# Kernel tuning notes

Hardware: AMD Instinct MI355X
Metric: run time of the kernel (lower is better)

Reference implementation:

```python
import jax, jax.numpy as jnp
import numpy as np

DIM = 512
HEADS = 8
DIM_HEAD = 64
LANDMARKS = 256  # dim // 2
PINV_ITERS = 6
KERNEL = 33  # residual conv kernel
NUM_LAYERS = 2
NUM_CLASSES = 2


def layernorm(x, g, b, eps=1e-5):
    mu = x.mean(-1, keepdims=True)
    var = ((x - mu) ** 2).mean(-1, keepdims=True)
    return (x - mu) * jax.lax.rsqrt(var + eps) * g + b


def moore_penrose_pinv(x, iters=PINV_ITERS):
    # x: (b, h, m, m); scaling uses GLOBAL max over all batch/heads (torch.max)
    abs_x = jnp.abs(x)
    col = abs_x.sum(-1).max()
    row = abs_x.sum(-2).max()
    z = jnp.swapaxes(x, -1, -2) / (col * row)
    I = jnp.eye(x.shape[-1], dtype=x.dtype)
    for _ in range(iters):
        xz = x @ z
        z = 0.25 * z @ (13. * I - xz @ (15. * I - xz @ (7. * I - xz)))
    return z


def nystrom_attention(x, w_qkv, w_out, b_out, conv_w):
    # x: (b, n, dim)
    b, n, _ = x.shape
    m = LANDMARKS
    pad = (m - n % m) % m
    if pad:
        x = jnp.pad(x, ((0, 0), (pad, 0), (0, 0)))  # pad at FRONT
    nf = n + pad
    qkv = x @ w_qkv  # (b, nf, 3*h*dh)
    qkv = qkv.reshape(b, nf, 3, HEADS, DIM_HEAD)
    q = jnp.transpose(qkv[:, :, 0], (0, 2, 1, 3)) * (DIM_HEAD ** -0.5)  # (b,h,nf,dh)
    k = jnp.transpose(qkv[:, :, 1], (0, 2, 1, 3))
    v = jnp.transpose(qkv[:, :, 2], (0, 2, 1, 3))
    l = nf // m
    q_l = q.reshape(b, HEADS, m, l, DIM_HEAD).mean(3)  # (b,h,m,dh)
    k_l = k.reshape(b, HEADS, m, l, DIM_HEAD).mean(3)
    sim1 = jnp.einsum('bhid,bhjd->bhij', q, k_l)      # (b,h,nf,m)
    sim2 = jnp.einsum('bhid,bhjd->bhij', q_l, k_l)    # (b,h,m,m)
    sim3 = jnp.einsum('bhid,bhjd->bhij', q_l, k)      # (b,h,m,nf)
    attn1 = jax.nn.softmax(sim1, axis=-1)
    attn2 = jax.nn.softmax(sim2, axis=-1)
    attn3 = jax.nn.softmax(sim3, axis=-1)
    attn2_inv = moore_penrose_pinv(attn2)
    out = (attn1 @ attn2_inv) @ (attn3 @ v)  # (b,h,nf,dh)
    # residual depthwise conv over sequence dim, per head (Conv2d groups=heads)
    res = jax.lax.conv_general_dilated(
        v, conv_w, window_strides=(1, 1), padding=((KERNEL // 2, KERNEL // 2), (0, 0)),
        dimension_numbers=('NCHW', 'OIHW', 'NCHW'), feature_group_count=HEADS)
    out = out + res
    out = jnp.transpose(out, (0, 2, 1, 3)).reshape(b, nf, HEADS * DIM_HEAD)
    out = out @ w_out + b_out
    return out[:, -n:]


def setup_inputs() -> dict:
    key = jax.random.key(0)
    ks = jax.random.split(key, 16)
    B, N = 2, 8191
    s = 0.02
    inp = {
        'h': jax.random.normal(ks[0], (B, N, 1024), jnp.float32),
        'w1': jax.random.normal(ks[1], (1024, DIM), jnp.float32) * s,
        'b1': jnp.zeros((DIM,), jnp.float32),
        'cls_token': jax.random.normal(ks[2], (1, 1, DIM), jnp.float32),
        'ln_g': jnp.ones((NUM_LAYERS, DIM), jnp.float32),
        'ln_b': jnp.zeros((NUM_LAYERS, DIM), jnp.float32),
        'w_qkv': jax.random.normal(ks[3], (NUM_LAYERS, DIM, 3 * HEADS * DIM_HEAD), jnp.float32) * s,
        'w_out': jax.random.normal(ks[4], (NUM_LAYERS, HEADS * DIM_HEAD, DIM), jnp.float32) * s,
        'b_out': jnp.zeros((NUM_LAYERS, DIM), jnp.float32),
        'conv_w': jax.random.normal(ks[5], (NUM_LAYERS, HEADS, 1, KERNEL, 1), jnp.float32) * s,
        'fn_g': jnp.ones((DIM,), jnp.float32),
        'fn_b': jnp.zeros((DIM,), jnp.float32),
        'w2': jax.random.normal(ks[6], (DIM, NUM_CLASSES), jnp.float32) * s,
        'b2': jnp.zeros((NUM_CLASSES,), jnp.float32),
    }
    return inp


def reference(h, w1, b1, cls_token, ln_g, ln_b, w_qkv, w_out, b_out, conv_w, fn_g, fn_b, w2, b2):
    x = jax.nn.relu(h @ w1 + b1)  # (B,N,512)
    B = x.shape[0]
    cls = jnp.broadcast_to(cls_token, (B, 1, DIM))
    x = jnp.concatenate([cls, x], axis=1)  # (B, N+1, 512)
    for i in range(NUM_LAYERS):
        x = x + nystrom_attention(layernorm(x, ln_g[i], ln_b[i]), w_qkv[i], w_out[i], b_out[i], conv_w[i])
    x = layernorm(x, fn_g, fn_b)[:, 0]
    logits = x @ w2 + b2
    return logits
```

## Files before the change

kernel.cpp:

```cpp
#include <hip/hip_runtime.h>
#include <hip/hip_bf16.h>

#define DIM 512
#define HEADS 8
#define DH 64
#define LM 256
#define NF 8192
#define BHN 16

typedef __attribute__((ext_vector_type(8))) short short8;
typedef __attribute__((ext_vector_type(4))) float f32x4;

__device__ __forceinline__ float bf2f(unsigned short u) {
  return __uint_as_float((unsigned)u << 16);
}
__device__ __forceinline__ unsigned short f2bf(float x) {
  unsigned u = __float_as_uint(x);
  unsigned r = u + 0x7fffu + ((u >> 16) & 1u);
  return (unsigned short)(r >> 16);
}

__device__ __forceinline__ void gl2lds16(const void* g, void* l) {
  __builtin_amdgcn_global_load_lds(
      (const __attribute__((address_space(1))) void*)g,
      (__attribute__((address_space(3))) void*)l, 16, 0, 0);
}

__device__ __forceinline__ void lds_fence() {
  asm volatile("s_waitcnt lgkmcnt(0)" ::: "memory");
  __builtin_amdgcn_sched_barrier(0);
}

__device__ __forceinline__ float waveReduceSum(float v) {
#pragma unroll
  for (int o = 1; o < 64; o <<= 1) v += __shfl_xor(v, o);
  return v;
}
__device__ __forceinline__ float waveReduceMax(float v) {
#pragma unroll
  for (int o = 1; o < 64; o <<= 1) v = fmaxf(v, __shfl_xor(v, o));
  return v;
}
__device__ __forceinline__ float blockReduceSum256(float v, float* sm) {
  v = waveReduceSum(v);
  int w = threadIdx.x >> 6;
  __syncthreads();
  if ((threadIdx.x & 63) == 0) sm[w] = v;
  __syncthreads();
  return sm[0] + sm[1] + sm[2] + sm[3];
}
__device__ __forceinline__ float blockReduceMax256(float v, float* sm) {
  v = waveReduceMax(v);
  int w = threadIdx.x >> 6;
  __syncthreads();
  if ((threadIdx.x & 63) == 0) sm[w] = v;
  __syncthreads();
  return fmaxf(fmaxf(sm[0], sm[1]), fmaxf(sm[2], sm[3]));
}

__global__ __launch_bounds__(256)
void cvt_bf16(const float* __restrict__ in, unsigned short* __restrict__ out,
              long long n) {
  long long i = ((long long)blockIdx.x * 256 + threadIdx.x) * 4;
  if (i + 3 < n) {
    float4 v = *(const float4*)&in[i];
    ushort4 o;
    o.x = f2bf(v.x); o.y = f2bf(v.y); o.z = f2bf(v.z); o.w = f2bf(v.w);
    *(ushort4*)&out[i] = o;
  } else {
    for (; i < n; i++) out[i] = f2bf(in[i]);
  }
}

__global__ __launch_bounds__(256)
void cvt_transpose(const float* __restrict__ in, unsigned short* __restrict__ out,
                   int Kd, int Nd) {
  __shared__ float t[32][33];
  int x = threadIdx.x & 31, y = threadIdx.x >> 5;
#pragma unroll
  for (int i = 0; i < 32; i += 8) {
    int k = blockIdx.y * 32 + y + i, n = blockIdx.x * 32 + x;
    t[y + i][x] = in[(long long)k * Nd + n];
  }
  __syncthreads();
#pragma unroll
  for (int i = 0; i < 32; i += 8) {
    int n = blockIdx.x * 32 + y + i, k = blockIdx.y * 32 + x;
    out[(long long)n * Kd + k] = f2bf(t[x][y + i]);
  }
}

__global__ __launch_bounds__(256)
void vt_transpose(const unsigned short* __restrict__ VB,
                  unsigned short* __restrict__ VT) {
  __shared__ unsigned short t[64][80];
  int bh = blockIdx.x >> 7, tile = blockIdx.x & 127;
  int n0 = tile * 64;
  int tid = threadIdx.x;
#pragma unroll
  for (int it = 0; it < 2; it++) {
    int s = it * 256 + tid;
    int nl = s >> 3, sg = s & 7;
    *(short8*)&t[nl][sg * 8] =
        *(const short8*)&VB[((long long)bh * NF + n0 + nl) * DH + sg * 8];
  }
  __syncthreads();
#pragma unroll
  for (int it = 0; it < 2; it++) {
    int s = it * 256 + tid;
    int dl = s >> 3, sg = s & 7;
    short8 v;
#pragma unroll
    for (int j = 0; j < 8; j++) ((unsigned short*)&v)[j] = t[sg * 8 + j][dl];
    *(short8*)&VT[((long long)bh * DH + dl) * NF + n0 + sg * 8] = v;
  }
}

__global__ __launch_bounds__(256) void write_cls(const float* __restrict__ cls,
                                                 float* __restrict__ X) {
  int t = blockIdx.x * 256 + threadIdx.x;
  int b = t >> 9, c = t & 511;
  X[(long long)b * NF * DIM + c] = cls[c];
}

#define MG_RELU 1
#define MG_ADDC 2
#define MG_BIAS 4
__global__ __launch_bounds__(256)
void gemm_mfma(const unsigned short* __restrict__ A,
               const unsigned short* __restrict__ B,
               const float* __restrict__ bias, float* __restrict__ C,
               unsigned short* __restrict__ qkv, unsigned short* __restrict__ vbuf,
               int M, int N, int K, int flags, int remap) {
  __shared__ short8 smem[1024];
  short8 (*Als)[64] = (short8 (*)[64])smem;
  short8 (*Bls)[64] = (short8 (*)[64])(smem + 512);
  const int tid = threadIdx.x;
  const int lane = tid & 63, wave = tid >> 6;
  const int wm = wave >> 1, wn = wave & 1;
  const int m0 = blockIdx.y * 128, n0 = blockIdx.x * 128;
  const int r16 = lane & 15, quad = lane >> 4;
  const unsigned short* pa0 = A + (long long)(m0 + 32 * wave + r16) * K + quad * 8;
  const unsigned short* pa1 = A + (long long)(m0 + 32 * wave + 16 + r16) * K + quad * 8;
  const unsigned short* pb0 = B + (long long)(n0 + 32 * wave + r16) * K + quad * 8;
  const unsigned short* pb1 = B + (long long)(n0 + 32 * wave + 16 + r16) * K + quad * 8;
  f32x4 acc[4][4] = {};
  for (int k0 = 0; k0 < K; k0 += 32) {
    gl2lds16(pa0, &Als[2 * wave][0]);
    gl2lds16(pa1, &Als[2 * wave + 1][0]);
    gl2lds16(pb0, &Bls[2 * wave][0]);
    gl2lds16(pb1, &Bls[2 * wave + 1][0]);
    pa0 += 32; pa1 += 32; pb0 += 32; pb1 += 32;
    __syncthreads();
    short8 af[4], bfr[4];
#pragma unroll
    for (int mt = 0; mt < 4; mt++) af[mt] = Als[wm * 4 + mt][lane];
#pragma unroll
    for (int nt = 0; nt < 4; nt++) bfr[nt] = Bls[wn * 4 + nt][lane];
#pragma unroll
    for (int mt = 0; mt < 4; mt++)
#pragma unroll
      for (int nt = 0; nt < 4; nt++)
        acc[mt][nt] = __builtin_amdgcn_mfma_f32_16x16x32_bf16(
            af[mt], bfr[nt], acc[mt][nt], 0, 0, 0);
    __syncthreads();
  }
  if (remap == 2) {
    unsigned short (*Ep)[32][64] = (unsigned short (*)[32][64])smem;
    int gn_base = n0 + wn * 64;
    int s = gn_base >> 9, hh = (gn_base >> 6) & 7;
    float scale = (s == 0) ? 0.125f : 1.f;
    unsigned short* basep =
        (s == 0) ? qkv : (s == 1) ? qkv + (long long)BHN * NF * DH : vbuf;
#pragma unroll
    for (int half = 0; half < 2; half++) {
      lds_fence();
#pragma unroll
      for (int mt = half * 2; mt < half * 2 + 2; mt++)
#pragma unroll
        for (int nt = 0; nt < 4; nt++)
#pragma unroll
          for (int r = 0; r < 4; r++)
            Ep[wave][(mt & 1) * 16 + quad * 4 + r][nt * 16 + r16] =
                f2bf(acc[mt][nt][r] * scale);
      lds_fence();
#pragma unroll
      for (int it = 0; it < 4; it++) {
        int idx = it * 64 + lane;
        int m_l = idx >> 3, sg = idx & 7;
        int gm = m0 + wm * 64 + half * 32 + m_l;
        int b = gm >> 13, n = gm & (NF - 1);
        int bh = b * HEADS + hh;
        short8 v = *(short8*)&Ep[wave][m_l][sg * 8];
        *(short8*)&basep[((long long)bh * NF + n) * DH + sg * 8] = v;
      }
    }
  } else {
#pragma unroll
    for (int mt = 0; mt < 4; mt++) {
#pragma unroll
      for (int nt = 0; nt < 4; nt++) {
#pragma unroll
        for (int r = 0; r < 4; r++) {
          int gm = m0 + wm * 64 + mt * 16 + quad * 4 + r;
          int gn = n0 + wn * 64 + nt * 16 + r16;
          if (gm >= M) continue;
          float v = acc[mt][nt][r];
          if (flags & MG_BIAS) v += bias[gn];
          long long idx;
          if (remap == 1) {
            int b = gm / 8191;
            int n = gm - b * 8191;
            idx = ((long long)(b * NF + 1 + n)) * DIM + gn;
          } else {
            idx = (long long)gm * N + gn;
          }
          if (flags & MG_ADDC) v += C[idx];
          if (flags & MG_RELU) v = fmaxf(v, 0.f);
          C[idx] = v;
        }
      }
    }
  }
}

__global__ __launch_bounds__(256)
void flash_attn1(const unsigned short* __restrict__ QB,
                 const unsigned short* __restrict__ KLB,
                 const unsigned short* __restrict__ WmB,
                 const unsigned short* __restrict__ XNC,
                 unsigned short* __restrict__ XNB2) {
  __shared__ unsigned short Plds[4][16][136];
  const int bh = blockIdx.y, b = bh >> 3, hh = bh & 7;
  const int tid = threadIdx.x, lane = tid & 63, wave = tid >> 6;
  const int r16 = lane & 15, quad = lane >> 4;
  const int m0w = blockIdx.x * 64 + wave * 16;
  const unsigned short* Aq = QB + (long long)bh * NF * DH;
  const unsigned short* Bk = KLB + (long long)bh * LM * DH;
  const unsigned short* Wm = WmB + (long long)bh * DH * LM;
  short8 af[2];
#pragma unroll
  for (int kc = 0; kc < 2; kc++)
    af[kc] = *(const short8*)&Aq[(long long)(m0w + r16) * DH + kc * 32 + quad * 8];
  short8 ones;
#pragma unroll
  for (int j = 0; j < 8; j++) ((unsigned short*)&ones)[j] = 0x3F80;
  f32x4 O[4] = {};
  f32x4 Ls = {};
#pragma unroll
  for (int t = 0; t < 2; t++) {
    int c0 = t * 128;
    f32x4 S[8] = {};
    __builtin_amdgcn_s_setprio(1);
#pragma unroll
    for (int nt = 0; nt < 8; nt++) {
#pragma unroll
      for (int kc = 0; kc < 2; kc++) {
        short8 bb = *(const short8*)&Bk[(long long)(c0 + nt * 16 + r16) * DH +
                                        kc * 32 + quad * 8];
        S[nt] = __builtin_amdgcn_mfma_f32_16x16x32_bf16(af[kc], bb, S[nt], 0, 0, 0);
      }
    }
    __builtin_amdgcn_s_setprio(0);
#pragma unroll
    for (int nt = 0; nt < 8; nt++)
#pragma unroll
      for (int r = 0; r < 4; r++)
        Plds[wave][quad * 4 + r][nt * 16 + r16] = f2bf(__expf(S[nt][r]));
    lds_fence();
    __builtin_amdgcn_s_setprio(1);
#pragma unroll
    for (int kc = 0; kc < 4; kc++) {
      short8 a = *(short8*)&Plds[wave][r16][kc * 32 + quad * 8];
      Ls = __builtin_amdgcn_mfma_f32_16x16x32_bf16(a, ones, Ls, 0, 0, 0);
#pragma unroll
      for (int nt2 = 0; nt2 < 4; nt2++) {
        short8 bb = *(const short8*)&Wm[(long long)(nt2 * 16 + r16) * LM + c0 +
                                        kc * 32 + quad * 8];
        O[nt2] = __builtin_amdgcn_mfma_f32_16x16x32_bf16(a, bb, O[nt2], 0, 0, 0);
      }
    }
    __builtin_amdgcn_s_setprio(0);
  }
  float invl[4];
#pragma unroll
  for (int r = 0; r < 4; r++) invl[r] = 1.f / Ls[r];
#pragma unroll
  for (int nt2 = 0; nt2 < 4; nt2++)
#pragma unroll
    for (int r = 0; r < 4; r++) {
      int row = m0w + quad * 4 + r;
      int d = nt2 * 16 + r16;
      long long gi = ((long long)(b * NF + row)) * DIM + hh * DH + d;
      XNB2[gi] = f2bf(O[nt2][r] * invl[r] + bf2f(XNC[gi]));
    }
}

__global__ __launch_bounds__(256)
void flash_attn3(const unsigned short* __restrict__ QLB,
                 const unsigned short* __restrict__ KB,
                 const unsigned short* __restrict__ VT,
                 float* __restrict__ Opart, float* __restrict__ Lpart) {
  __shared__ unsigned short Plds[4][16][136];
  const int bh = blockIdx.z, ks = blockIdx.y;
  const int tid = threadIdx.x, lane = tid & 63, wave = tid >> 6;
  const int r16 = lane & 15, quad = lane >> 4;
  const int m0w = blockIdx.x * 64 + wave * 16;
  const unsigned short* Aq = QLB + (long long)bh * LM * DH;
  const unsigned short* Bk = KB + (long long)bh * NF * DH;
  const unsigned short* Vt = VT + (long long)bh * DH * NF;
  short8 af[2];
#pragma unroll
  for (int kc = 0; kc < 2; kc++)
    af[kc] = *(const short8*)&Aq[(long long)(m0w + r16) * DH + kc * 32 + quad * 8];
  short8 ones;
#pragma unroll
  for (int j = 0; j < 8; j++) ((unsigned short*)&ones)[j] = 0x3F80;
  f32x4 O[4] = {};
  f32x4 Ls = {};
  for (int t = 0; t < 4; t++) {
    int kv0 = ks * 512 + t * 128;
    f32x4 S[8] = {};
    __builtin_amdgcn_s_setprio(1);
#pragma unroll
    for (int nt = 0; nt < 8; nt++) {
#pragma unroll
      for (int kc = 0; kc < 2; kc++) {
        short8 bb = *(const short8*)&Bk[(long long)(kv0 + nt * 16 + r16) * DH +
                                        kc * 32 + quad * 8];
        S[nt] = __builtin_amdgcn_mfma_f32_16x16x32_bf16(af[kc], bb, S[nt], 0, 0, 0);
      }
    }
    __builtin_amdgcn_s_setprio(0);
#pragma unroll
    for (int nt = 0; nt < 8; nt++)
#pragma unroll
      for (int r = 0; r < 4; r++)
        Plds[wave][quad * 4 + r][nt * 16 + r16] = f2bf(__expf(S[nt][r]));
    lds_fence();
    __builtin_amdgcn_s_setprio(1);
#pragma unroll
    for (int kc2 = 0; kc2 < 4; kc2++) {
      short8 a = *(short8*)&Plds[wave][r16][kc2 * 32 + quad * 8];
      Ls = __builtin_amdgcn_mfma_f32_16x16x32_bf16(a, ones, Ls, 0, 0, 0);
#pragma unroll
      for (int nt2 = 0; nt2 < 4; nt2++) {
        short8 bb = *(const short8*)&Vt[(long long)(nt2 * 16 + r16) * NF + kv0 +
                                        kc2 * 32 + quad * 8];
        O[nt2] = __builtin_amdgcn_mfma_f32_16x16x32_bf16(a, bb, O[nt2], 0, 0, 0);
      }
    }
    __builtin_amdgcn_s_setprio(0);
  }
  float* Ob = Opart + (((long long)ks * BHN + bh) * LM) * DH;
#pragma unroll
  for (int nt2 = 0; nt2 < 4; nt2++)
#pragma unroll
    for (int r = 0; r < 4; r++) {
      int row = m0w + quad * 4 + r;
      Ob[(long long)row * DH + nt2 * 16 + r16] = O[nt2][r];
    }
  if (r16 == 0) {
#pragma unroll
    for (int r = 0; r < 4; r++) {
      int row = m0w + quad * 4 + r;
      Lpart[((long long)ks * BHN + bh) * LM + row] = Ls[r];
    }
  }
}

__global__ __launch_bounds__(256)
void attn3_merge(const float* __restrict__ Opart, const float* __restrict__ Lpart,
                 float* __restrict__ O3) {
  int idx = blockIdx.x * 256 + threadIdx.x;
  int bh = idx >> 14, rem = idx & 16383;
  int row = rem >> 6, d = rem & 63;
  float L = 0.f, acc = 0.f;
#pragma unroll
  for (int c = 0; c < 16; c++) {
    L += Lpart[((long long)c * BHN + bh) * LM + row];
    acc += Opart[(((long long)c * BHN + bh) * LM + row) * DH + d];
  }
  O3[((long long)bh * LM + row) * DH + d] = acc / L;
}

__global__ __launch_bounds__(256)
void zinit(const float* __restrict__ a2, const unsigned* __restrict__ red,
           unsigned short* __restrict__ zn, unsigned short* __restrict__ zt) {
  float scale = 1.0f / __uint_as_float(red[1]);
  long long idx = (long long)blockIdx.x * 256 + threadIdx.x;
  int bh = (int)(idx >> 16);
  int ij = (int)(idx & 65535);
  int i = ij >> 8, j = ij & 255;
  zn[idx] = f2bf(a2[((long long)bh << 16) + (j << 8) + i] * scale);
  zt[idx] = f2bf(a2[idx] * scale);
}

#define PV_CN 1
#define PV_CT 2
#define PV_CF 4
#define PV_ID 8
__global__ __launch_bounds__(256)
void pinv_bf(const unsigned short* __restrict__ An,
             const unsigned short* __restrict__ Bt,
             unsigned short* __restrict__ Cn, unsigned short* __restrict__ Ct,
             float* __restrict__ Cf, float alpha, float ident, float beta,
             int flags) {
  __shared__ unsigned short Als[32][256];
  __shared__ unsigned short Bls[32][256];
  const int batch = blockIdx.z;
  An += (long long)batch * 65536;
  Bt += (long long)batch * 65536;
  const int tid = threadIdx.x, lane = tid & 63, wave = tid >> 6;
  const int wm2 = wave >> 1, wn2 = wave & 1;
  const int m0 = blockIdx.y * 32, n0 = blockIdx.x * 32;
  const int r16 = lane & 15, quad = lane >> 4;
#pragma unroll
  for (int j = 0; j < 4; j++) {
    int g = (j * 4 + wave) * 64 + lane;
    int row = g >> 5, plog = (g & 31) ^ (row & 7);
    gl2lds16(An + ((m0 + row) << 8) + plog * 8,
             (char*)Als + (j * 4 + wave) * 1024);
    gl2lds16(Bt + ((n0 + row) << 8) + plog * 8,
             (char*)Bls + (j * 4 + wave) * 1024);
  }
  __syncthreads();
  f32x4 acc = {};
  const int arow = wm2 * 16 + r16, brow = wn2 * 16 + r16;
#pragma unroll
  for (int kk = 0; kk < 8; kk++) {
    short8 af = *(const short8*)((const char*)Als + arow * 512 +
                                 ((kk * 4 + quad) ^ (arow & 7)) * 16);
    short8 bfr = *(const short8*)((const char*)Bls + brow * 512 +
                                  ((kk * 4 + quad) ^ (brow & 7)) * 16);
    acc = __builtin_amdgcn_mfma_f32_16x16x32_bf16(af, bfr, acc, 0, 0, 0);
  }
  long long cb = (long long)batch * 65536;
  int ncol = n0 + wn2 * 16 + r16;
  float vals[4];
#pragma unroll
  for (int r = 0; r < 4; r++) {
    int mrow = wm2 * 16 + quad * 4 + r;
    float v = beta * acc[r];
    if (flags & PV_ID) {
      unsigned short a = *(const unsigned short*)(
          (const char*)Als + mrow * 512 +
          (((ncol >> 3) ^ (mrow & 7)) * 16) + (ncol & 7) * 2);
      v += ident * bf2f(a);
    }
    vals[r] = v * alpha;
    int gm = m0 + mrow;
    if (flags & PV_CN) Cn[cb + ((long long)gm << 8) + ncol] = f2bf(vals[r]);
    if (flags & PV_CF) Cf[cb + ((long long)gm << 8) + ncol] = vals[r];
  }
  if (flags & PV_CT) {
    ushort4 o;
    o.x = f2bf(vals[0]); o.y = f2bf(vals[1]);
    o.z = f2bf(vals[2]); o.w = f2bf(vals[3]);
    *(ushort4*)&Ct[cb + ((long long)ncol << 8) + m0 + wm2 * 16 + quad * 4] = o;
  }
}

#define BG_BIDENT 16
__global__ __launch_bounds__(256)
void bgemm(const float* __restrict__ A, const float* __restrict__ B,
           float* __restrict__ C, int M, int N, int K,
           long long sA, long long sB, long long sC,
           float alpha, float ident, int flags) {
  const int batch = blockIdx.z;
  A += (long long)batch * sA;
  B += (long long)batch * sB;
  float* Cb = C + (long long)batch * sC;
  __shared__ float As[16][68];
  __shared__ float Bs[16][68];
  const int tid = threadIdx.x;
  const int tx = tid & 15, ty = tid >> 4;
  const int m0 = blockIdx.y * 64, n0 = blockIdx.x * 64;
  float acc[4][4] = {};
  for (int k0 = 0; k0 < K; k0 += 16) {
    {
      int k = tid & 15;
      int mBase = tid >> 4;
#pragma unroll
      for (int i = 0; i < 4; i++) {
        int m = mBase + i * 16;
        int gm = m0 + m;
        As[k][m] = (gm < M) ? A[(long long)gm * K + (k0 + k)] : 0.f;
      }
    }
    {
      int n = tid & 63;
      int kBase = tid >> 6;
#pragma unroll
      for (int i = 0; i < 4; i++) {
        int k = kBase + i * 4;
        int gn = n0 + n;
        float vb = (gn < N) ? B[(long long)(k0 + k) * N + gn] : 0.f;
        if (flags & BG_BIDENT) vb = ident * ((k0 + k) == gn ? 1.f : 0.f) - vb;
        Bs[k][n] = vb;
      }
    }
    __syncthreads();
#pragma unroll
    for (int k = 0; k < 16; k++) {
      float a[4], b[4];
#pragma unroll
      for (int i = 0; i < 4; i++) a[i] = As[k][ty * 4 + i];
#pragma unroll
      for (int j = 0; j < 4; j++) b[j] = Bs[k][tx * 4 + j];
#pragma unroll
      for (int i = 0; i < 4; i++)
#pragma unroll
        for (int j = 0; j < 4; j++) acc[i][j] = fmaf(a[i], b[j], acc[i][j]);
    }
    __syncthreads();
  }
#pragma unroll
  for (int i = 0; i < 4; i++) {
    int gm = m0 + ty * 4 + i;
    if (gm >= M) continue;
#pragma unroll
    for (int j = 0; j < 4; j++) {
      int gn = n0 + tx * 4 + j;
      if (gn >= N) continue;
      Cb[(long long)gm * N + gn] = alpha * acc[i][j];
    }
  }
}

__global__ __launch_bounds__(256)
void wm_gemm(const float* __restrict__ Z, const float* __restrict__ O3,
             unsigned short* __restrict__ WmT) {
  const int batch = blockIdx.y;
  const int m0 = blockIdx.x * 64;
  const float* A = Z + (long long)batch * 65536;
  const float* B = O3 + (long long)batch * LM * DH;
  __shared__ float As[16][68];
  __shared__ float Bs[16][68];
  const int tid = threadIdx.x, tx = tid & 15, ty = tid >> 4;
  float acc[4][4] = {};
  for (int k0 = 0; k0 < 256; k0 += 16) {
    {
      int k = tid & 15, mB = tid >> 4;
#pragma unroll
      for (int i = 0; i < 4; i++) {
        int m = mB + i * 16;
        As[k][m] = A[(long long)(m0 + m) * 256 + k0 + k];
      }
    }
    {
      int n = tid & 63, kB = tid >> 6;
#pragma unroll
      for (int i = 0; i < 4; i++) {
        int k = kB + i * 4;
        Bs[k][n] = B[(long long)(k0 + k) * DH + n];
      }
    }
    __syncthreads();
#pragma unroll
    for (int k = 0; k < 16; k++) {
      float a[4], b[4];
#pragma unroll
      for (int i = 0; i < 4; i++) a[i] = As[k][ty * 4 + i];
#pragma unroll
      for (int j = 0; j < 4; j++) b[j] = Bs[k][tx * 4 + j];
#pragma unroll
      for (int i = 0; i < 4; i++)
#pragma unroll
        for (int j = 0; j < 4; j++) acc[i][j] = fmaf(a[i], b[j], acc[i][j]);
    }
    __syncthreads();
  }
#pragma unroll
  for (int i = 0; i < 4; i++)
#pragma unroll
    for (int j = 0; j < 4; j++)
      WmT[((long long)batch * DH + tx * 4 + j) * LM + m0 + ty * 4 + i] =
          f2bf(acc[i][j]);
}

__global__ __launch_bounds__(256)
void layernorm_rows_bf16(const float* __restrict__ X, const float* __restrict__ g,
                         const float* __restrict__ bt,
                         unsigned short* __restrict__ Y) {
  __shared__ float sm[4];
  long long r = blockIdx.x;
  const float* x = X + r * DIM;
  int t = threadIdx.x;
  float v0 = x[t], v1 = x[t + 256];
  float mu = blockReduceSum256(v0 + v1, sm) * (1.f / DIM);
  float d0 = v0 - mu, d1 = v1 - mu;
  float var = blockReduceSum256(d0 * d0 + d1 * d1, sm) * (1.f / DIM);
  float rs = 1.0f / sqrtf(var + 1e-5f);
  unsigned short* y = Y + r * DIM;
  y[t] = f2bf(d0 * rs * g[t] + bt[t]);
  y[t + 256] = f2bf(d1 * rs * g[t + 256] + bt[t + 256]);
}

__global__ __launch_bounds__(64)
void landmarks_k(const unsigned short* __restrict__ q,
                 const unsigned short* __restrict__ k,
                 float* __restrict__ ql, float* __restrict__ kl,
                 unsigned short* __restrict__ qlb,
                 unsigned short* __restrict__ klb) {
  int bh = blockIdx.x >> 8, i = blockIdx.x & 255, d = threadIdx.x;
  long long base = ((long long)bh * NF + i * 32) * DH + d;
  float sq = 0.f, sk = 0.f;
#pragma unroll 4
  for (int l = 0; l < 32; l++) {
    sq += bf2f(q[base + (long long)l * DH]);
    sk += bf2f(k[base + (long long)l * DH]);
  }
  long long o = ((long long)bh * LM + i) * DH + d;
  float mq = sq * (1.f / 32.f), mk = sk * (1.f / 32.f);
  ql[o] = mq; kl[o] = mk;
  qlb[o] = f2bf(mq); klb[o] = f2bf(mk);
}

__global__ __launch_bounds__(256)
void sim2_softmax(const float* __restrict__ ql, const float* __restrict__ kl,
                  float* __restrict__ a2, unsigned short* __restrict__ a2b) {
  __shared__ float qs[64];
  __shared__ float sm[4];
  int bh = blockIdx.x >> 8, i = blockIdx.x & 255, t = threadIdx.x;
  if (t < 64) qs[t] = ql[((long long)bh * LM + i) * DH + t];
  __syncthreads();
  const float* krow = kl + (long long)bh * LM * DH + (long long)t * DH;
  float s = 0.f;
#pragma unroll
  for (int d = 0; d < 64; d++) s += qs[d] * krow[d];
  float m = blockReduceMax256(s, sm);
  float e = expf(s - m);
  float sum = blockReduceSum256(e, sm);
  long long off = ((long long)bh * LM + i) * LM + t;
  float v = e / sum;
  a2[off] = v;
  a2b[off] = f2bf(v);
}

__global__ __launch_bounds__(256)
void pinv_reduce(const float* __restrict__ a2, unsigned* __restrict__ red) {
  __shared__ float sm[4];
  int bh = blockIdx.x, t = threadIdx.x;
  const float* A = a2 + (long long)bh * LM * LM;
  float cs = 0.f;
  for (int i = 0; i < 256; i++) cs += fabsf(A[i * 256 + t]);
  float cm = blockReduceMax256(cs, sm);
  if (t == 0) atomicMax(&red[1], __float_as_uint(cm));
}

__global__ __launch_bounds__(256)
void conv_res_bf16(const unsigned short* __restrict__ vt,
                   const float* __restrict__ cw,
                   unsigned short* __restrict__ out) {
  int bh = blockIdx.x >> 6, tile = blockIdx.x & 63;
  int b = bh >> 3, hh = bh & 7;
  int t = threadIdx.x;
  int d = t & 63, pg = t >> 6;
  float wr[33];
#pragma unroll
  for (int kk = 0; kk < 33; kk++) wr[kk] = cw[hh * 33 + kk];
  const unsigned short* src = &vt[((long long)bh * DH + d) * NF];
  int base = tile * 128 + pg * 32;
  int n0 = base - 16;
  float win[64];
#pragma unroll
  for (int jj = 0; jj < 8; jj++) {
    int c = n0 + jj * 8;
    if (c >= 0 && c + 7 < NF) {
      short8 v = *(const short8*)&src[c];
#pragma unroll
      for (int j = 0; j < 8; j++)
        win[jj * 8 + j] = bf2f((unsigned short)v[j]);
    } else {
#pragma unroll
      for (int j = 0; j < 8; j++) {
        int nn = c + j;
        win[jj * 8 + j] = (nn >= 0 && nn < NF) ? bf2f(src[nn]) : 0.f;
      }
    }
  }
  unsigned short* dst = &out[((long long)(b * NF + base)) * DIM + hh * DH + d];
#pragma unroll
  for (int p = 0; p < 32; p++) {
    float s = 0.f;
#pragma unroll
    for (int kk = 0; kk < 33; kk++) s = fmaf(wr[kk], win[p + kk], s);
    dst[(long long)p * DIM] = f2bf(s);
  }
}

__global__ __launch_bounds__(256)
void final_head(const float* __restrict__ X, const float* __restrict__ g,
                const float* __restrict__ bt, const float* __restrict__ w2,
                const float* __restrict__ b2, float* __restrict__ out) {
  __shared__ float sm[4];
  int b = blockIdx.x, t = threadIdx.x;
  const float* row = X + (long long)b * NF * DIM;
  float v0 = row[t], v1 = row[t + 256];
  float mu = blockReduceSum256(v0 + v1, sm) * (1.f / DIM);
  float d0 = v0 - mu, d1 = v1 - mu;
  float var = blockReduceSum256(d0 * d0 + d1 * d1, sm) * (1.f / DIM);
  float rs = 1.0f / sqrtf(var + 1e-5f);
  float y0 = d0 * rs * g[t] + bt[t];
  float y1 = d1 * rs * g[t + 256] + bt[t + 256];
  float l0 = y0 * w2[t * 2 + 0] + y1 * w2[(t + 256) * 2 + 0];
  float l1 = y0 * w2[t * 2 + 1] + y1 * w2[(t + 256) * 2 + 1];
  l0 = blockReduceSum256(l0, sm);
  l1 = blockReduceSum256(l1, sm);
  if (t == 0) {
    out[b * 2 + 0] = l0 + b2[0];
    out[b * 2 + 1] = l1 + b2[1];
  }
}

extern "C" void kernel_launch(void* const* d_in, const int* in_sizes, int n_in,
                              void* d_out, int out_size, void* d_ws,
                              size_t ws_size, hipStream_t stream) {
  const float* h      = (const float*)d_in[0];
  const float* w1     = (const float*)d_in[1];
  const float* b1     = (const float*)d_in[2];
  const float* cls    = (const float*)d_in[3];
  const float* ln_g   = (const float*)d_in[4];
  const float* ln_b   = (const float*)d_in[5];
  const float* w_qkv  = (const float*)d_in[6];
  const float* w_out  = (const float*)d_in[7];
  const float* b_out  = (const float*)d_in[8];
  const float* conv_w = (const float*)d_in[9];
  const float* fn_g   = (const float*)d_in[10];
  const float* fn_b   = (const float*)d_in[11];
  const float* w2     = (const float*)d_in[12];
  const float* b2     = (const float*)d_in[13];

  float* ws = (float*)d_ws;
  const long long XSZ = (long long)2 * NF * DIM;
  const long long QSZ = (long long)BHN * NF * DH;
  float* X  = ws;
  unsigned short* STAGE = (unsigned short*)(X + XSZ);
  unsigned short* HB   = STAGE;
  unsigned short* XNB1 = STAGE;
  unsigned short* XNB2 = STAGE;
  unsigned short* VB   = STAGE + XSZ;
  unsigned short* XNC  = STAGE + XSZ;
  unsigned short* QB = STAGE + 2 * XSZ;
  unsigned short* KB = QB + QSZ;
  unsigned short* VT = KB + QSZ;
  float* QL = (float*)(VT + QSZ);
  float* KL = QL + 262144;
  unsigned short* QLB = (unsigned short*)(KL + 262144);
  unsigned short* KLB = QLB + 262144;
  float* A2 = (float*)(KLB + 262144);
  float* ZA = A2 + 1048576;
  float* ZB = ZA + 1048576;
  float* P  = ZB + 1048576;
  float* T1 = P + 1048576;
  float* T2 = T1 + 1048576;
  float* Mpart = T2 + 1048576;
  float* Lpart = Mpart + 65536;
  float* O3 = Lpart + 65536;
  unsigned short* WmB = (unsigned short*)(O3 + 262144);
  unsigned* RED = (unsigned*)(WmB + 262144);
  unsigned short* WT = (unsigned short*)(RED + 4);
  unsigned short* W1T = WT;
  unsigned short* WQ0 = W1T + 524288;
  unsigned short* WQ1 = WQ0 + 786432;
  unsigned short* WO0 = WQ1 + 786432;
  unsigned short* WO1 = WO0 + 262144;

  unsigned short* A2B = VB;
  float* Opart = (float*)VB;
  unsigned short* Zan = (unsigned short*)P;
  unsigned short* Zat = Zan + 1048576;
  unsigned short* Zbn = (unsigned short*)ZB;
  unsigned short* Zbt = Zbn + 1048576;
  unsigned short* Pn  = (unsigned short*)T1;
  unsigned short* Pt  = Pn + 1048576;
  unsigned short* T1t = (unsigned short*)T2;
  unsigned short* T2t = T1t + 1048576;

  write_cls<<<4, 256, 0, stream>>>(cls, X);
  cvt_bf16<<<16382, 256, 0, stream>>>(h, HB, (long long)16382 * 1024);
  cvt_transpose<<<dim3(512 / 32, 1024 / 32), 256, 0, stream>>>(w1, W1T, 1024, 512);
  cvt_transpose<<<dim3(1536 / 32, 512 / 32), 256, 0, stream>>>(w_qkv, WQ0, 512, 1536);
  cvt_transpose<<<dim3(1536 / 32, 512 / 32), 256, 0, stream>>>(
      w_qkv + (long long)DIM * 1536, WQ1, 512, 1536);
  cvt_transpose<<<dim3(512 / 32, 512 / 32), 256, 0, stream>>>(w_out, WO0, 512, 512);
  cvt_transpose<<<dim3(512 / 32, 512 / 32), 256, 0, stream>>>(
      w_out + (long long)DIM * DIM, WO1, 512, 512);
  gemm_mfma<<<dim3(4, 128), 256, 0, stream>>>(HB, W1T, b1, X, nullptr, nullptr,
                                              16382, 512, 1024, MG_RELU | MG_BIAS, 1);

  for (int L = 0; L < 2; L++) {
    layernorm_rows_bf16<<<2 * NF, 256, 0, stream>>>(X, ln_g + L * DIM,
                                                    ln_b + L * DIM, XNB1);
    gemm_mfma<<<dim3(12, 128), 256, 0, stream>>>(XNB1, L ? WQ1 : WQ0, nullptr,
                                                 nullptr, QB, VB, 16384, 1536,
                                                 512, 0, 2);
    vt_transpose<<<BHN * 128, 256, 0, stream>>>(VB, VT);

    landmarks_k<<<BHN * LM, 64, 0, stream>>>(QB, KB, QL, KL, QLB, KLB);
    sim2_softmax<<<BHN * LM, 256, 0, stream>>>(QL, KL, A2, A2B);
    hipMemsetAsync(RED, 0, 16, stream);
    pinv_reduce<<<BHN, 256, 0, stream>>>(A2, RED);
    zinit<<<4096, 256, 0, stream>>>(A2, RED, Zan, Zat);
    for (int it = 0; it < 5; it++) {
      const unsigned short* zcn = (it & 1) ? Zbn : Zan;
      const unsigned short* zct = (it & 1) ? Zbt : Zat;
      unsigned short* znn = (it & 1) ? Zan : Zbn;
      unsigned short* znt = (it & 1) ? Zat : Zbt;
      pinv_bf<<<dim3(8, 8, BHN), 256, 0, stream>>>(
          A2B, zct, Pn, Pt, nullptr, 1.f, 0.f, 1.f, PV_CN | PV_CT);
      pinv_bf<<<dim3(8, 8, BHN), 256, 0, stream>>>(
          Pn, Pt, nullptr, T1t, nullptr, 1.f, 7.f, -1.f, PV_CT | PV_ID);
      pinv_bf<<<dim3(8, 8, BHN), 256, 0, stream>>>(
          Pn, T1t, nullptr, T2t, nullptr, 1.f, 15.f, -1.f, PV_CT | PV_ID);
      if (it < 4)
        pinv_bf<<<dim3(8, 8, BHN), 256, 0, stream>>>(
            zcn, T2t, znn, znt, nullptr, 0.25f, 13.f, -1.f,
            PV_CN | PV_CT | PV_ID);
      else
        pinv_bf<<<dim3(8, 8, BHN), 256, 0, stream>>>(
            zcn, T2t, nullptr, nullptr, ZB, 0.25f, 13.f, -1.f, PV_CF | PV_ID);
    }
    bgemm<<<dim3(4, 4, BHN), 256, 0, stream>>>(A2, ZB, P, 256, 256, 256,
                                               65536, 65536, 65536, 1.f, 0.f, 0);
    bgemm<<<dim3(4, 4, BHN), 256, 0, stream>>>(P, P, T1, 256, 256, 256,
                                               65536, 65536, 65536, 1.f, 7.f,
                                               BG_BIDENT);
    bgemm<<<dim3(4, 4, BHN), 256, 0, stream>>>(P, T1, T2, 256, 256, 256,
                                               65536, 65536, 65536, 1.f, 15.f,
                                               BG_BIDENT);
    bgemm<<<dim3(4, 4, BHN), 256, 0, stream>>>(ZB, T2, ZA, 256, 256, 256,
                                               65536, 65536, 65536, 0.25f,
                                               13.f, BG_BIDENT);

    flash_attn3<<<dim3(4, 16, BHN), 256, 0, stream>>>(QLB, KB, VT, Opart, Lpart);
    attn3_merge<<<1024, 256, 0, stream>>>(Opart, Lpart, O3);

    wm_gemm<<<dim3(4, BHN), 256, 0, stream>>>(ZA, O3, WmB);

    conv_res_bf16<<<BHN * 64, 256, 0, stream>>>(VT, conv_w + L * 264, XNC);

    flash_attn1<<<dim3(128, BHN), 256, 0, stream>>>(QB, KLB, WmB, XNC, XNB2);

    gemm_mfma<<<dim3(4, 128), 256, 0, stream>>>(XNB2, L ? WO1 : WO0,
                                                b_out + L * DIM, X, nullptr,
                                                nullptr, 16384, 512, 512,
                                                MG_ADDC | MG_BIAS, 0);
  }
  final_head<<<2, 256, 0, stream>>>(X, fn_g, fn_b, w2, b2, (float*)d_out);
}
```

Baseline: 1.437 ms.

## Stage K/V and landmark tiles in swizzled LDS for both flash attention kernels

flash_attn1 now copies the per-head landmark keys and Wm matrix into XOR-swizzled LDS once per block. It uses 512-thread blocks that each cover 256 query rows, instead of every wave reading K and Wm from global memory. flash_attn3 double-buffers 128-row K and V^T tiles through LDS using async global-to-LDS loads, and each block handles all 256 landmark rows for one key split. Both changes aim to cut redundant global and L2 traffic and improve reuse, at the cost of larger LDS footprint, fewer blocks, and extra block-wide barriers.

```diff
diff --git a/kernel.cpp b/kernel.cpp
--- a/kernel.cpp
+++ b/kernel.cpp
@@ -224,148 +224,209 @@
   }
 }
 
-__global__ __launch_bounds__(256)
+__global__ __launch_bounds__(512)
 void flash_attn1(const unsigned short* __restrict__ QB,
                  const unsigned short* __restrict__ KLB,
                  const unsigned short* __restrict__ WmB,
                  const unsigned short* __restrict__ XNC,
                  unsigned short* __restrict__ XNB2) {
-  __shared__ unsigned short Plds[4][16][136];
+  __shared__ unsigned short Klds[LM * DH];
+  __shared__ unsigned short Wlds[DH * LM];
+  __shared__ unsigned short Plds[8][16][136];
   const int bh = blockIdx.y, b = bh >> 3, hh = bh & 7;
   const int tid = threadIdx.x, lane = tid & 63, wave = tid >> 6;
   const int r16 = lane & 15, quad = lane >> 4;
-  const int m0w = blockIdx.x * 64 + wave * 16;
   const unsigned short* Aq = QB + (long long)bh * NF * DH;
-  const unsigned short* Bk = KLB + (long long)bh * LM * DH;
-  const unsigned short* Wm = WmB + (long long)bh * DH * LM;
-  short8 af[2];
-#pragma unroll
-  for (int kc = 0; kc < 2; kc++)
-    af[kc] = *(const short8*)&Aq[(long long)(m0w + r16) * DH + kc * 32 + quad * 8];
+  const unsigned short* Kg = KLB + (long long)bh * LM * DH;
+  const unsigned short* Wg = WmB + (long long)bh * DH * LM;
+#pragma unroll
+  for (int j = 0; j < 4; j++) {
+    int u = j * 8 + wave;
+    int s = u * 64 + lane;
+    int row = s >> 3, ck = s & 7;
+    gl2lds16(Kg + row * DH + ((ck ^ (row & 7)) << 3), (char*)Klds + u * 1024);
+  }
+#pragma unroll
+  for (int j = 0; j < 4; j++) {
+    int u = j * 8 + wave;
+    int s = u * 64 + lane;
+    int row = s >> 5, ck = s & 31;
+    gl2lds16(Wg + row * LM + ((ck ^ (row & 7)) << 3), (char*)Wlds + u * 1024);
+  }
+  __syncthreads();
   short8 ones;
 #pragma unroll
   for (int j = 0; j < 8; j++) ((unsigned short*)&ones)[j] = 0x3F80;
-  f32x4 O[4] = {};
-  f32x4 Ls = {};
-#pragma unroll
-  for (int t = 0; t < 2; t++) {
-    int c0 = t * 128;
-    f32x4 S[8] = {};
-    __builtin_amdgcn_s_setprio(1);
-#pragma unroll
-    for (int nt = 0; nt < 8; nt++) {
-#pragma unroll
-      for (int kc = 0; kc < 2; kc++) {
-        short8 bb = *(const short8*)&Bk[(long long)(c0 + nt * 16 + r16) * DH +
-                                        kc * 32 + quad * 8];
-        S[nt] = __builtin_amdgcn_mfma_f32_16x16x32_bf16(af[kc], bb, S[nt], 0, 0, 0);
-      }
-    }
-    __builtin_amdgcn_s_setprio(0);
-#pragma unroll
-    for (int nt = 0; nt < 8; nt++)
-#pragma unroll
-      for (int r = 0; r < 4; r++)
-        Plds[wave][quad * 4 + r][nt * 16 + r16] = f2bf(__expf(S[nt][r]));
-    lds_fence();
-    __builtin_amdgcn_s_setprio(1);
-#pragma unroll
-    for (int kc = 0; kc < 4; kc++) {
-      short8 a = *(short8*)&Plds[wave][r16][kc * 32 + quad * 8];
-      Ls = __builtin_amdgcn_mfma_f32_16x16x32_bf16(a, ones, Ls, 0, 0, 0);
-#pragma unroll
-      for (int nt2 = 0; nt2 < 4; nt2++) {
-        short8 bb = *(const short8*)&Wm[(long long)(nt2 * 16 + r16) * LM + c0 +
-                                        kc * 32 + quad * 8];
-        O[nt2] = __builtin_amdgcn_mfma_f32_16x16x32_bf16(a, bb, O[nt2], 0, 0, 0);
-      }
-    }
-    __builtin_amdgcn_s_setprio(0);
-  }
-  float invl[4];
-#pragma unroll
-  for (int r = 0; r < 4; r++) invl[r] = 1.f / Ls[r];
-#pragma unroll
-  for (int nt2 = 0; nt2 < 4; nt2++)
-#pragma unroll
-    for (int r = 0; r < 4; r++) {
-      int row = m0w + quad * 4 + r;
-      int d = nt2 * 16 + r16;
-      long long gi = ((long long)(b * NF + row)) * DIM + hh * DH + d;
-      XNB2[gi] = f2bf(O[nt2][r] * invl[r] + bf2f(XNC[gi]));
-    }
-}
-
-__global__ __launch_bounds__(256)
+#pragma unroll
+  for (int rt = 0; rt < 2; rt++) {
+    const int m0w = blockIdx.x * 256 + (wave * 2 + rt) * 16;
+    short8 af[2];
+#pragma unroll
+    for (int kc = 0; kc < 2; kc++)
+      af[kc] = *(const short8*)&Aq[(long long)(m0w + r16) * DH + kc * 32 + quad * 8];
+    f32x4 O[4] = {};
+    f32x4 Ls = {};
+#pragma unroll
+    for (int t = 0; t < 2; t++) {
+      int c0 = t * 128;
+      f32x4 S[8] = {};
+      __builtin_amdgcn_s_setprio(1);
+#pragma unroll
+      for (int nt = 0; nt < 8; nt++) {
+        int kl = c0 + nt * 16 + r16;
+#pragma unroll
+        for (int kc = 0; kc < 2; kc++) {
+          short8 bb = *(const short8*)((const char*)Klds + kl * 128 +
+                                       (((kc * 4 + quad) ^ (kl & 7)) << 4));
+          S[nt] = __builtin_amdgcn_mfma_f32_16x16x32_bf16(af[kc], bb, S[nt], 0, 0, 0);
+        }
+      }
+      __builtin_amdgcn_s_setprio(0);
+#pragma unroll
+      for (int nt = 0; nt < 8; nt++)
+#pragma unroll
+        for (int r = 0; r < 4; r++)
+          Plds[wave][quad * 4 + r][nt * 16 + r16] = f2bf(__expf(S[nt][r]));
+      lds_fence();
+      __builtin_amdgcn_s_setprio(1);
+#pragma unroll
+      for (int kc = 0; kc < 4; kc++) {
+        short8 a = *(short8*)&Plds[wave][r16][kc * 32 + quad * 8];
+        Ls = __builtin_amdgcn_mfma_f32_16x16x32_bf16(a, ones, Ls, 0, 0, 0);
+#pragma unroll
+        for (int nt2 = 0; nt2 < 4; nt2++) {
+          int wrow = nt2 * 16 + r16;
+          int cu = (c0 >> 3) + kc * 4 + quad;
+          short8 bb = *(const short8*)((const char*)Wlds + wrow * 512 +
+                                       ((cu ^ (wrow & 7)) << 4));
+          O[nt2] = __builtin_amdgcn_mfma_f32_16x16x32_bf16(a, bb, O[nt2], 0, 0, 0);
+        }
+      }
+      __builtin_amdgcn_s_setprio(0);
+    }
+    float invl[4];
+#pragma unroll
+    for (int r = 0; r < 4; r++) invl[r] = 1.f / Ls[r];
+#pragma unroll
+    for (int nt2 = 0; nt2 < 4; nt2++)
+#pragma unroll
+      for (int r = 0; r < 4; r++) {
+        int row = m0w + quad * 4 + r;
+        int d = nt2 * 16 + r16;
+        long long gi = ((long long)(b * NF + row)) * DIM + hh * DH + d;
+        XNB2[gi] = f2bf(O[nt2][r] * invl[r] + bf2f(XNC[gi]));
+      }
+  }
+}
+
+__device__ __forceinline__ void stage_kv3(const unsigned short* Kg,
+                                          const unsigned short* Vg,
+                                          unsigned short* Kb, unsigned short* Vb,
+                                          int kv0, int wave, int lane) {
+#pragma unroll
+  for (int j = 0; j < 2; j++) {
+    int u = j * 8 + wave;
+    int s = u * 64 + lane;
+    int kr = s >> 3, kc = s & 7;
+    gl2lds16(Kg + (long long)(kv0 + kr) * DH + ((kc ^ (kr & 7)) << 3),
+             (char*)Kb + u * 1024);
+    int vr = s >> 4, vc = s & 15;
+    gl2lds16(Vg + (long long)vr * NF + kv0 + ((vc ^ (vr & 7)) << 3),
+             (char*)Vb + u * 1024);
+  }
+}
+
+__global__ __launch_bounds__(512)
 void flash_attn3(const unsigned short* __restrict__ QLB,
                  const unsigned short* __restrict__ KB,
                  const unsigned short* __restrict__ VT,
                  float* __restrict__ Opart, float* __restrict__ Lpart) {
-  __shared__ unsigned short Plds[4][16][136];
-  const int bh = blockIdx.z, ks = blockIdx.y;
+  __shared__ unsigned short Klds[2][128 * DH];
+  __shared__ unsigned short Vlds[2][DH * 128];
+  __shared__ unsigned short Plds[8][16][136];
+  const int ks = blockIdx.x, bh = blockIdx.y;
   const int tid = threadIdx.x, lane = tid & 63, wave = tid >> 6;
   const int r16 = lane & 15, quad = lane >> 4;
-  const int m0w = blockIdx.x * 64 + wave * 16;
   const unsigned short* Aq = QLB + (long long)bh * LM * DH;
-  const unsigned short* Bk = KB + (long long)bh * NF * DH;
-  const unsigned short* Vt = VT + (long long)bh * DH * NF;
-  short8 af[2];
-#pragma unroll
-  for (int kc = 0; kc < 2; kc++)
-    af[kc] = *(const short8*)&Aq[(long long)(m0w + r16) * DH + kc * 32 + quad * 8];
+  const unsigned short* Kg = KB + (long long)bh * NF * DH;
+  const unsigned short* Vg = VT + (long long)bh * DH * NF;
+  short8 af2[2][2];
+#pragma unroll
+  for (int rt = 0; rt < 2; rt++) {
+    int m0w = (wave * 2 + rt) * 16;
+#pragma unroll
+    for (int kc = 0; kc < 2; kc++)
+      af2[rt][kc] =
+          *(const short8*)&Aq[(long long)(m0w + r16) * DH + kc * 32 + quad * 8];
+  }
   short8 ones;
 #pragma unroll
   for (int j = 0; j < 8; j++) ((unsigned short*)&ones)[j] = 0x3F80;
-  f32x4 O[4] = {};
-  f32x4 Ls = {};
+  f32x4 O2[2][4] = {};
+  f32x4 Ls2[2] = {};
+  stage_kv3(Kg, Vg, Klds[0], Vlds[0], ks * 512, wave, lane);
+  __syncthreads();
   for (int t = 0; t < 4; t++) {
-    int kv0 = ks * 512 + t * 128;
-    f32x4 S[8] = {};
-    __builtin_amdgcn_s_setprio(1);
-#pragma unroll
-    for (int nt = 0; nt < 8; nt++) {
-#pragma unroll
-      for (int kc = 0; kc < 2; kc++) {
-        short8 bb = *(const short8*)&Bk[(long long)(kv0 + nt * 16 + r16) * DH +
-                                        kc * 32 + quad * 8];
-        S[nt] = __builtin_amdgcn_mfma_f32_16x16x32_bf16(af[kc], bb, S[nt], 0, 0, 0);
-      }
-    }
-    __builtin_amdgcn_s_setprio(0);
-#pragma unroll
-    for (int nt = 0; nt < 8; nt++)
+    int cb = t & 1;
+    if (t < 3)
+      stage_kv3(Kg, Vg, Klds[cb ^ 1], Vlds[cb ^ 1], ks * 512 + (t + 1) * 128,
+                wave, lane);
+    const unsigned short* Kb = Klds[cb];
+    const unsigned short* Vb = Vlds[cb];
+#pragma unroll
+    for (int rt = 0; rt < 2; rt++) {
+      f32x4 S[8] = {};
+      __builtin_amdgcn_s_setprio(1);
+#pragma unroll
+      for (int nt = 0; nt < 8; nt++) {
+        int kl = nt * 16 + r16;
+#pragma unroll
+        for (int kc = 0; kc < 2; kc++) {
+          short8 bb = *(const short8*)((const char*)Kb + kl * 128 +
+                                       (((kc * 4 + quad) ^ (kl & 7)) << 4));
+          S[nt] = __builtin_amdgcn_mfma_f32_16x16x32_bf16(af2[rt][kc], bb, S[nt],
+                                                          0, 0, 0);
+        }
+      }
+      __builtin_amdgcn_s_setprio(0);
+#pragma unroll
+      for (int nt = 0; nt < 8; nt++)
+#pragma unroll
+        for (int r = 0; r < 4; r++)
+          Plds[wave][quad * 4 + r][nt * 16 + r16] = f2bf(__expf(S[nt][r]));
+      lds_fence();
+      __builtin_amdgcn_s_setprio(1);
+#pragma unroll
+      for (int kc2 = 0; kc2 < 4; kc2++) {
+        short8 a = *(short8*)&Plds[wave][r16][kc2 * 32 + quad * 8];
+        Ls2[rt] = __builtin_amdgcn_mfma_f32_16x16x32_bf16(a, ones, Ls2[rt], 0, 0, 0);
+#pragma unroll
+        for (int nt2 = 0; nt2 < 4; nt2++) {
+          int vr = nt2 * 16 + r16;
+          int u = kc2 * 4 + quad;
+          short8 bb = *(const short8*)((const char*)Vb + vr * 256 +
+                                       ((u ^ (vr & 7)) << 4));
+          O2[rt][nt2] = __builtin_amdgcn_mfma_f32_16x16x32_bf16(a, bb, O2[rt][nt2],
+                                                                0, 0, 0);
+        }
+      }
+      __builtin_amdgcn_s_setprio(0);
+    }
+    __syncthreads();
+  }
+  float* Ob = Opart + (((long long)ks * BHN + bh) * LM) * DH;
+#pragma unroll
+  for (int rt = 0; rt < 2; rt++) {
+    int m0w = (wave * 2 + rt) * 16;
+#pragma unroll
+    for (int nt2 = 0; nt2 < 4; nt2++)
 #pragma unroll
       for (int r = 0; r < 4; r++)
-        Plds[wave][quad * 4 + r][nt * 16 + r16] = f2bf(__expf(S[nt][r]));
-    lds_fence();
-    __builtin_amdgcn_s_setprio(1);
-#pragma unroll
-    for (int kc2 = 0; kc2 < 4; kc2++) {
-      short8 a = *(short8*)&Plds[wave][r16][kc2 * 32 + quad * 8];
-      Ls = __builtin_amdgcn_mfma_f32_16x16x32_bf16(a, ones, Ls, 0, 0, 0);
-#pragma unroll
-      for (int nt2 = 0; nt2 < 4; nt2++) {
-        short8 bb = *(const short8*)&Vt[(long long)(nt2 * 16 + r16) * NF + kv0 +
-                                        kc2 * 32 + quad * 8];
-        O[nt2] = __builtin_amdgcn_mfma_f32_16x16x32_bf16(a, bb, O[nt2], 0, 0, 0);
-      }
-    }
-    __builtin_amdgcn_s_setprio(0);
-  }
-  float* Ob = Opart + (((long long)ks * BHN + bh) * LM) * DH;
-#pragma unroll
-  for (int nt2 = 0; nt2 < 4; nt2++)
-#pragma unroll
-    for (int r = 0; r < 4; r++) {
-      int row = m0w + quad * 4 + r;
-      Ob[(long long)row * DH + nt2 * 16 + r16] = O[nt2][r];
-    }
-  if (r16 == 0) {
-#pragma unroll
-    for (int r = 0; r < 4; r++) {
-      int row = m0w + quad * 4 + r;
-      Lpart[((long long)ks * BHN + bh) * LM + row] = Ls[r];
-    }
+        Ob[(long long)(m0w + quad * 4 + r) * DH + nt2 * 16 + r16] = O2[rt][nt2][r];
+    if (r16 == 0)
+#pragma unroll
+      for (int r = 0; r < 4; r++)
+        Lpart[((long long)ks * BHN + bh) * LM + m0w + quad * 4 + r] = Ls2[rt][r];
   }
 }
 
@@ -834,14 +895,14 @@
                                                65536, 65536, 65536, 0.25f,
                                                13.f, BG_BIDENT);
 
-    flash_attn3<<<dim3(4, 16, BHN), 256, 0, stream>>>(QLB, KB, VT, Opart, Lpart);
+    flash_attn3<<<dim3(16, BHN), 512, 0, stream>>>(QLB, KB, VT, Opart, Lpart);
     attn3_merge<<<1024, 256, 0, stream>>>(Opart, Lpart, O3);
 
     wm_gemm<<<dim3(4, BHN), 256, 0, stream>>>(ZA, O3, WmB);
 
     conv_res_bf16<<<BHN * 64, 256, 0, stream>>>(VT, conv_w + L * 264, XNC);
 
-    flash_attn1<<<dim3(128, BHN), 256, 0, stream>>>(QB, KLB, WmB, XNC, XNB2);
+    flash_attn1<<<dim3(32, BHN), 512, 0, stream>>>(QB, KLB, WmB, XNC, XNB2);
 
     gemm_mfma<<<dim3(4, 128), 256, 0, stream>>>(XNB2, L ? WO1 : WO0,
                                                 b_out + L * DIM, X, nullptr,
```

New measurement: 1.266 ms. 11.9% less time.
